# Kernel tuning notes

Measured on AMD Instinct MI355X. Metric: run time of the kernel, lower is better.

## Reference

```python
import jax, jax.numpy as jnp
import numpy as np

OUT, N_GROUPS, GROUP = 11008, 32, 128
IN = N_GROUPS * GROUP  # 4096
TOKENS = 2048


def setup_inputs() -> dict:
    key = jax.random.key(0)
    k_x, k_w, k_sc, k_s, k_b = jax.random.split(key, 5)
    x = jax.random.normal(k_x, (TOKENS, IN), dtype=jnp.float32)
    # quantized 4-bit signed weights in [-7, 7] (stored int8 in torch; int32 here)
    w_q = jax.random.randint(k_w, (OUT, N_GROUPS, GROUP), -7, 8, dtype=jnp.int32)
    # per-(out, group) positive scales, bounded away from zero like the clamp(min=1e-5)
    scales = jax.random.uniform(k_sc, (OUT, N_GROUPS, 1), dtype=jnp.float32, minval=1e-3, maxval=0.05)
    # smoothing vector: positive, bounded away from zero (it divides x)
    s = jax.random.uniform(k_s, (IN,), dtype=jnp.float32, minval=0.5, maxval=2.0)
    bias = jax.random.normal(k_b, (OUT,), dtype=jnp.float32)
    return {"x": x, "w_q": w_q, "scales": scales, "s": s, "bias": bias}


def reference(x, w_q, scales, s, bias):
    orig_dtype = x.dtype
    # group-wise dequant: [O, G, K] * [O, G, 1] -> [O, I]
    w_recon = (w_q.astype(jnp.float32) * scales).reshape(OUT, IN)
    x_f = x.astype(jnp.float32) / s  # smoothing-scale division
    y = x_f @ w_recon.T + bias
    return y.astype(orig_dtype)
```

## Files before the change

### kernel.cpp

```cpp
#include <hip/hip_runtime.h>
#include <hip/hip_bf16.h>

#define TOKENS  2048
#define IN_DIM  4096
#define OUT_DIM 11008
#define NGROUPS 32

#define BM 128
#define BN 128
#define BKB 128
#define THREADS 512
#define NKT   (IN_DIM / BKB)
#define BUFB  32768
#define BOFF  16384

#define PREPA_BLOCKS  TOKENS
#define PREPB_BLOCKS  (OUT_DIM * IN_DIM / 16 / 256)
#define PREPSC_BLOCKS (OUT_DIM * NGROUPS / 256)
#define PREP_GRID     (PREPA_BLOCKS + PREPB_BLOCKS + PREPSC_BLOCKS)

using f32x4  = __attribute__((ext_vector_type(4))) float;
using i32x4  = __attribute__((ext_vector_type(4))) int;
using bf16x8 = __attribute__((ext_vector_type(8))) short;

typedef __attribute__((address_space(3))) char as3c;

static __device__ __forceinline__ short f2bf(float f) {
    union { float f; unsigned u; } v; v.f = f;
    unsigned r = v.u + 0x7FFFu + ((v.u >> 16) & 1u);
    return (short)(r >> 16);
}

static __device__ __forceinline__ int pack4(int a, int b, int c, int d) {
    return (a & 255) | ((b & 255) << 8) | ((c & 255) << 16) | ((d & 255) << 24);
}

#define SB0 __builtin_amdgcn_sched_barrier(0)
#define LDSR(dst, addr)   asm volatile("ds_read_b128 %0, %1" : "=v"(dst) : "v"(addr))
#define WAITL(n) do { asm volatile("s_waitcnt lgkmcnt(" #n ")"); SB0; } while (0)
#define WAITV(n) do { asm volatile("s_waitcnt vmcnt(" #n ")");  SB0; } while (0)

__global__ __launch_bounds__(256) void prep_fused(
    const float* __restrict__ x, const int* __restrict__ wq,
    const float* __restrict__ scales, const float* __restrict__ s,
    char* __restrict__ Aq, float* __restrict__ sx,
    char* __restrict__ Bq, float* __restrict__ scT)
{
    __shared__ float wm[4];
    const int bid = blockIdx.x, t = threadIdx.x;

    if (bid < PREPA_BLOCKS) {
        const int row = bid;
        const float* xp = x + (size_t)row * IN_DIM + t * 16;
        const float* sp = s + t * 16;
        f32x4 v[4];
        float m = 0.f;
        #pragma unroll
        for (int q = 0; q < 4; ++q) {
            f32x4 xv = *(const f32x4*)(xp + q * 4);
            f32x4 sv = *(const f32x4*)(sp + q * 4);
            #pragma unroll
            for (int e = 0; e < 4; ++e) {
                v[q][e] = xv[e] / sv[e];
                m = fmaxf(m, fabsf(v[q][e]));
            }
        }
        #pragma unroll
        for (int off = 32; off; off >>= 1) m = fmaxf(m, __shfl_xor(m, off));
        if ((t & 63) == 0) wm[t >> 6] = m;
        __syncthreads();
        m = fmaxf(fmaxf(wm[0], wm[1]), fmaxf(wm[2], wm[3]));
        m = fmaxf(m, 1e-20f);
        const float inv = 127.0f / m;
        i32x4 pk;
        #pragma unroll
        for (int q = 0; q < 4; ++q)
            pk[q] = pack4((int)rintf(v[q][0] * inv), (int)rintf(v[q][1] * inv),
                          (int)rintf(v[q][2] * inv), (int)rintf(v[q][3] * inv));
        ((i32x4*)(Aq + (size_t)row * IN_DIM))[t] = pk;
        if (t == 0) sx[row] = m * (1.0f / 127.0f);
    } else if (bid < PREPA_BLOCKS + PREPB_BLOCKS) {
        const int idx = (bid - PREPA_BLOCKS) * 256 + t;
        const int* wp = wq + (size_t)idx * 16;
        i32x4 w0 = *(const i32x4*)wp, w1 = *(const i32x4*)(wp + 4);
        i32x4 w2 = *(const i32x4*)(wp + 8), w3 = *(const i32x4*)(wp + 12);
        i32x4 pk;
        pk[0] = pack4(w0[0], w0[1], w0[2], w0[3]);
        pk[1] = pack4(w1[0], w1[1], w1[2], w1[3]);
        pk[2] = pack4(w2[0], w2[1], w2[2], w2[3]);
        pk[3] = pack4(w3[0], w3[1], w3[2], w3[3]);
        ((i32x4*)Bq)[idx] = pk;
    } else {
        const int idx = (bid - PREPA_BLOCKS - PREPB_BLOCKS) * 256 + t;
        const int g = idx / OUT_DIM;
        const int o = idx - g * OUT_DIM;
        scT[idx] = scales[o * NGROUPS + g];
    }
}

__global__ __launch_bounds__(THREADS, 4) void awq_gemm_i8(
    const char* __restrict__ Aq, const char* __restrict__ Bq,
    const float* __restrict__ scT, const float* __restrict__ sx,
    const float* __restrict__ bias, float* __restrict__ out)
{
    const int rb = blockIdx.x;
    const int bm = (rb >> 3) & 15;
    const int bn = (((rb >> 3) >> 4) << 3) + (rb & 7);
    if (bn >= OUT_DIM / BN) return;

    __shared__ char smem[2 * BUFB];
    as3c* ldsb = (as3c*)smem;
    const unsigned lbase = (unsigned)(size_t)ldsb;

    const int tid  = threadIdx.x;
    const int lane = tid & 63;
    const int w    = tid >> 6;
    const int wr   = w >> 2;
    const int wc   = w & 3;
    const int fr   = lane & 15;
    const int fko  = lane >> 4;

    const int h7 = fr & 7;
    const unsigned swz0 = (unsigned)(((0 * 4 + fko) ^ h7) * 16);
    const unsigned swz1 = (unsigned)(((1 * 4 + fko) ^ h7) * 16);
    const unsigned aB0 = lbase + (wr * 64 + fr) * 128 + swz0;
    const unsigned aB1 = lbase + (wr * 64 + fr) * 128 + swz1;
    const unsigned bB0 = lbase + BOFF + (wc * 32 + fr) * 128 + swz0;
    const unsigned bB1 = lbase + BOFF + (wc * 32 + fr) * 128 + swz1;

    const int srow = tid >> 3;
    const int sg   = ((tid & 7) ^ (srow & 7)) * 16;
    const char* aSrc = Aq + (size_t)(bm * BM + srow) * IN_DIM + sg;
    const char* bSrc = Bq + (size_t)(bn * BN + srow) * IN_DIM + sg;

    const float* scp = scT + bn * BN + wc * 32 + fr;

#define STG_A(Q, KT, P) __builtin_amdgcn_global_load_lds( \
    (const __attribute__((address_space(1))) void*)(const void*)(aSrc + (size_t)((Q) * 64) * IN_DIM + (KT) * BKB), \
    (__attribute__((address_space(3))) void*)(ldsb + (P) * BUFB + (Q) * 8192 + tid * 16), 16, 0, 0)
#define STG_B(Q, KT, P) __builtin_amdgcn_global_load_lds( \
    (const __attribute__((address_space(1))) void*)(const void*)(bSrc + (size_t)((Q) * 64) * IN_DIM + (KT) * BKB), \
    (__attribute__((address_space(3))) void*)(ldsb + (P) * BUFB + BOFF + (Q) * 8192 + tid * 16), 16, 0, 0)

#define SCV_GLOAD(D0, D1, G) do { \
    asm volatile("global_load_dword %0, %1, off" : "=v"(D0) : "v"(scp + (size_t)(G) * OUT_DIM)); \
    asm volatile("global_load_dword %0, %1, off" : "=v"(D1) : "v"(scp + (size_t)(G) * OUT_DIM + 16)); \
    SB0; } while (0)

    f32x4 accf[4][2];
    #pragma unroll
    for (int i = 0; i < 4; ++i) {
        accf[i][0] = (f32x4){0.f, 0.f, 0.f, 0.f};
        accf[i][1] = (f32x4){0.f, 0.f, 0.f, 0.f};
    }

    float c0, c1, n0 = 0.f, n1 = 0.f;

    STG_A(0, 0, 0); STG_A(1, 0, 0); STG_B(0, 0, 0); STG_B(1, 0, 0);
    SCV_GLOAD(c0, c1, 0);
    STG_A(0, 1, 1); STG_A(1, 1, 1); STG_B(0, 1, 1); STG_B(1, 1, 1);
    WAITV(4);
    __builtin_amdgcn_s_barrier();
    SB0;

    for (int t = 0; t < NKT; ++t) {
        const int P = t & 1;
        const unsigned po = (unsigned)(P * BUFB);
        const bool haveN = (t + 1 < NKT);
        const bool haveS = (t + 2 < NKT);

        i32x4 a[4][2], b[2][2];
        LDSR(b[0][0], bB0 + po);        LDSR(b[0][1], bB1 + po);
        LDSR(b[1][0], bB0 + po + 2048); LDSR(b[1][1], bB1 + po + 2048);
        #pragma unroll
        for (int i = 0; i < 4; ++i) {
            LDSR(a[i][0], aB0 + po + i * 2048);
            LDSR(a[i][1], aB1 + po + i * 2048);
        }
        WAITL(0);
        __builtin_amdgcn_s_barrier();
        SB0;

        if (haveN) SCV_GLOAD(n0, n1, t + 1);
        if (haveS) { STG_A(0, t + 2, P); STG_A(1, t + 2, P);
                     STG_B(0, t + 2, P); STG_B(1, t + 2, P); }

        __builtin_amdgcn_s_setprio(1);
        #pragma unroll
        for (int i = 0; i < 4; ++i) {
            i32x4 t0 = __builtin_amdgcn_mfma_i32_16x16x64_i8(a[i][0], b[0][0], (i32x4){0,0,0,0}, 0, 0, 0);
            t0       = __builtin_amdgcn_mfma_i32_16x16x64_i8(a[i][1], b[0][1], t0, 0, 0, 0);
            i32x4 t1 = __builtin_amdgcn_mfma_i32_16x16x64_i8(a[i][0], b[1][0], (i32x4){0,0,0,0}, 0, 0, 0);
            t1       = __builtin_amdgcn_mfma_i32_16x16x64_i8(a[i][1], b[1][1], t1, 0, 0, 0);
            #pragma unroll
            for (int e = 0; e < 4; ++e) {
                accf[i][0][e] += (float)t0[e] * c0;
                accf[i][1][e] += (float)t1[e] * c1;
            }
        }
        __builtin_amdgcn_s_setprio(0);

        if (t < NKT - 2) { WAITV(4); } else { WAITV(0); }
        __builtin_amdgcn_s_barrier();
        SB0;
        if (haveN) { c0 = n0; c1 = n1; }
    }

    #pragma unroll
    for (int i = 0; i < 4; ++i) {
        const int row = bm * BM + wr * 64 + i * 16 + fko * 4;
        const f32x4 sxv = *(const f32x4*)(sx + row);
        #pragma unroll
        for (int j = 0; j < 2; ++j) {
            const int col = bn * BN + wc * 32 + j * 16 + fr;
            const float bv = bias[col];
            #pragma unroll
            for (int e = 0; e < 4; ++e)
                out[(size_t)(row + e) * OUT_DIM + col] = accf[i][j][e] * sxv[e] + bv;
        }
    }

#undef STG_A
#undef STG_B
#undef SCV_GLOAD
}

__global__ __launch_bounds__(256) void awq_gemm_fb(
    const float* __restrict__ x, const int* __restrict__ wq,
    const float* __restrict__ scales, const float* __restrict__ s,
    const float* __restrict__ bias, float* __restrict__ out)
{
    __shared__ short As[128][32];
    __shared__ short Bs[128][32];
    const int tid = threadIdx.x, lane = tid & 63, wave = tid >> 6;
    const int nbn = OUT_DIM / 128;
    const int bm = blockIdx.x / nbn, bn = blockIdx.x % nbn;
    const int srow = tid >> 1, scol = (tid & 1) * 16;
    const int wm = (wave >> 1) * 64, wn = (wave & 1) * 64;
    f32x4 acc[4][4];
    #pragma unroll
    for (int i = 0; i < 4; ++i)
        #pragma unroll
        for (int j = 0; j < 4; ++j) acc[i][j] = (f32x4){0.f, 0.f, 0.f, 0.f};
    const float* xrow = x + (size_t)(bm * 128 + srow) * IN_DIM;
    const int* wrow = wq + (size_t)(bn * 128 + srow) * IN_DIM;
    const float* scrow = scales + (size_t)(bn * 128 + srow) * NGROUPS;
    const int fr = lane & 15, fk = (lane >> 4) * 8, fq = lane >> 4;
    for (int kt = 0; kt < IN_DIM / 32; ++kt) {
        const int k0 = kt * 32;
        {
            const float* xp = xrow + k0 + scol;
            const float* sp = s + k0 + scol;
            short tmp[16];
            #pragma unroll
            for (int q = 0; q < 4; ++q) {
                f32x4 xv = *(const f32x4*)(xp + q * 4);
                f32x4 sv = *(const f32x4*)(sp + q * 4);
                #pragma unroll
                for (int e = 0; e < 4; ++e) tmp[q * 4 + e] = f2bf(xv[e] / sv[e]);
            }
            #pragma unroll
            for (int e = 0; e < 16; ++e) As[srow][scol + e] = tmp[e];
        }
        {
            const float sc = scrow[kt >> 2];
            const int* wp = wrow + k0 + scol;
            short tmp[16];
            #pragma unroll
            for (int q = 0; q < 4; ++q) {
                i32x4 wv = *(const i32x4*)(wp + q * 4);
                #pragma unroll
                for (int e = 0; e < 4; ++e) tmp[q * 4 + e] = f2bf((float)wv[e] * sc);
            }
            #pragma unroll
            for (int e = 0; e < 16; ++e) Bs[srow][scol + e] = tmp[e];
        }
        __syncthreads();
        bf16x8 a[4], b[4];
        #pragma unroll
        for (int i = 0; i < 4; ++i) a[i] = *(const bf16x8*)&As[wm + i * 16 + fr][fk];
        #pragma unroll
        for (int j = 0; j < 4; ++j) b[j] = *(const bf16x8*)&Bs[wn + j * 16 + fr][fk];
        #pragma unroll
        for (int i = 0; i < 4; ++i)
            #pragma unroll
            for (int j = 0; j < 4; ++j)
                acc[i][j] = __builtin_amdgcn_mfma_f32_16x16x32_bf16(a[i], b[j], acc[i][j], 0, 0, 0);
        __syncthreads();
    }
    #pragma unroll
    for (int i = 0; i < 4; ++i) {
        const int row = bm * 128 + wm + i * 16 + fq * 4;
        #pragma unroll
        for (int j = 0; j < 4; ++j) {
            const int col = bn * 128 + wn + j * 16 + fr;
            const float bv = bias[col];
            #pragma unroll
            for (int e = 0; e < 4; ++e)
                out[(size_t)(row + e) * OUT_DIM + col] = acc[i][j][e] + bv;
        }
    }
}

extern "C" void kernel_launch(void* const* d_in, const int* in_sizes, int n_in,
                              void* d_out, int out_size, void* d_ws, size_t ws_size,
                              hipStream_t stream) {
    const float* x      = (const float*)d_in[0];
    const int*   wq     = (const int*)  d_in[1];
    const float* scales = (const float*)d_in[2];
    const float* s      = (const float*)d_in[3];
    const float* bias   = (const float*)d_in[4];
    float* out = (float*)d_out;

    const size_t off_sx = (size_t)TOKENS * IN_DIM;
    const size_t off_bq = off_sx + 8192;
    const size_t off_sc = off_bq + (size_t)OUT_DIM * IN_DIM;
    const size_t need   = off_sc + (size_t)OUT_DIM * NGROUPS * 4;

    if (ws_size >= need) {
        char*  Aq  = (char*)d_ws;
        float* sxw = (float*)((char*)d_ws + off_sx);
        char*  Bq  = (char*)d_ws + off_bq;
        float* scT = (float*)((char*)d_ws + off_sc);
        prep_fused<<<PREP_GRID, 256, 0, stream>>>(x, wq, scales, s, Aq, sxw, Bq, scT);
        awq_gemm_i8<<<1408, THREADS, 0, stream>>>(Aq, Bq, scT, sxw, bias, out);
    } else {
        awq_gemm_fb<<<(TOKENS / 128) * (OUT_DIM / 128), 256, 0, stream>>>(x, wq, scales, s, bias, out);
    }
}
```

Measured before the change: 174.6 us.

## Use 256-thread blocks with 64x64 wave tiles and single-buffered LDS

Halves the block to four waves, so each wave now computes a 64x64 output sub-tile with four B fragments instead of two. This raises register-level reuse of the A fragments and cuts LDS reads per MFMA. LDS drops from a double buffer to a single 32KB buffer. The next tile is fetched straight into that buffer once the current tile is in registers, and a full vmcnt wait ends each iteration. The cost is a shallower prefetch pipeline and more accumulator registers per thread, with launch bounds lowered to 3 blocks.

```diff
diff --git a/kernel.cpp b/kernel.cpp
--- a/kernel.cpp
+++ b/kernel.cpp
@@ -9,7 +9,7 @@
 #define BM 128
 #define BN 128
 #define BKB 128
-#define THREADS 512
+#define THREADS 256
 #define NKT   (IN_DIM / BKB)
 #define BUFB  32768
 #define BOFF  16384
@@ -98,7 +98,7 @@
     }
 }
 
-__global__ __launch_bounds__(THREADS, 4) void awq_gemm_i8(
+__global__ __launch_bounds__(THREADS, 3) void awq_gemm_i8(
     const char* __restrict__ Aq, const char* __restrict__ Bq,
     const float* __restrict__ scT, const float* __restrict__ sx,
     const float* __restrict__ bias, float* __restrict__ out)
@@ -108,15 +108,15 @@
     const int bn = (((rb >> 3) >> 4) << 3) + (rb & 7);
     if (bn >= OUT_DIM / BN) return;
 
-    __shared__ char smem[2 * BUFB];
+    __shared__ char smem[BUFB];
     as3c* ldsb = (as3c*)smem;
     const unsigned lbase = (unsigned)(size_t)ldsb;
 
     const int tid  = threadIdx.x;
     const int lane = tid & 63;
     const int w    = tid >> 6;
-    const int wr   = w >> 2;
-    const int wc   = w & 3;
+    const int wr   = w >> 1;
+    const int wc   = w & 1;
     const int fr   = lane & 15;
     const int fko  = lane >> 4;
 
@@ -125,85 +125,89 @@
     const unsigned swz1 = (unsigned)(((1 * 4 + fko) ^ h7) * 16);
     const unsigned aB0 = lbase + (wr * 64 + fr) * 128 + swz0;
     const unsigned aB1 = lbase + (wr * 64 + fr) * 128 + swz1;
-    const unsigned bB0 = lbase + BOFF + (wc * 32 + fr) * 128 + swz0;
-    const unsigned bB1 = lbase + BOFF + (wc * 32 + fr) * 128 + swz1;
+    const unsigned bB0 = lbase + BOFF + (wc * 64 + fr) * 128 + swz0;
+    const unsigned bB1 = lbase + BOFF + (wc * 64 + fr) * 128 + swz1;
 
     const int srow = tid >> 3;
     const int sg   = ((tid & 7) ^ (srow & 7)) * 16;
     const char* aSrc = Aq + (size_t)(bm * BM + srow) * IN_DIM + sg;
     const char* bSrc = Bq + (size_t)(bn * BN + srow) * IN_DIM + sg;
 
-    const float* scp = scT + bn * BN + wc * 32 + fr;
-
-#define STG_A(Q, KT, P) __builtin_amdgcn_global_load_lds( \
-    (const __attribute__((address_space(1))) void*)(const void*)(aSrc + (size_t)((Q) * 64) * IN_DIM + (KT) * BKB), \
-    (__attribute__((address_space(3))) void*)(ldsb + (P) * BUFB + (Q) * 8192 + tid * 16), 16, 0, 0)
-#define STG_B(Q, KT, P) __builtin_amdgcn_global_load_lds( \
-    (const __attribute__((address_space(1))) void*)(const void*)(bSrc + (size_t)((Q) * 64) * IN_DIM + (KT) * BKB), \
-    (__attribute__((address_space(3))) void*)(ldsb + (P) * BUFB + BOFF + (Q) * 8192 + tid * 16), 16, 0, 0)
-
-#define SCV_GLOAD(D0, D1, G) do { \
-    asm volatile("global_load_dword %0, %1, off" : "=v"(D0) : "v"(scp + (size_t)(G) * OUT_DIM)); \
-    asm volatile("global_load_dword %0, %1, off" : "=v"(D1) : "v"(scp + (size_t)(G) * OUT_DIM + 16)); \
+    const float* scp = scT + bn * BN + wc * 64 + fr;
+
+#define STG_A(Q, KT) __builtin_amdgcn_global_load_lds( \
+    (const __attribute__((address_space(1))) void*)(const void*)(aSrc + (size_t)((Q) * 32) * IN_DIM + (KT) * BKB), \
+    (__attribute__((address_space(3))) void*)(ldsb + (Q) * 4096 + tid * 16), 16, 0, 0)
+#define STG_B(Q, KT) __builtin_amdgcn_global_load_lds( \
+    (const __attribute__((address_space(1))) void*)(const void*)(bSrc + (size_t)((Q) * 32) * IN_DIM + (KT) * BKB), \
+    (__attribute__((address_space(3))) void*)(ldsb + BOFF + (Q) * 4096 + tid * 16), 16, 0, 0)
+#define STG_TILE(KT) do { \
+    STG_A(0, KT); STG_A(1, KT); STG_A(2, KT); STG_A(3, KT); \
+    STG_B(0, KT); STG_B(1, KT); STG_B(2, KT); STG_B(3, KT); \
     SB0; } while (0)
 
-    f32x4 accf[4][2];
+#define SCV4(D0, D1, D2, D3, G) do { \
+    asm volatile("global_load_dword %0, %1, off"            : "=v"(D0) : "v"(scp + (size_t)(G) * OUT_DIM)); \
+    asm volatile("global_load_dword %0, %1, off offset:64"  : "=v"(D1) : "v"(scp + (size_t)(G) * OUT_DIM)); \
+    asm volatile("global_load_dword %0, %1, off offset:128" : "=v"(D2) : "v"(scp + (size_t)(G) * OUT_DIM)); \
+    asm volatile("global_load_dword %0, %1, off offset:192" : "=v"(D3) : "v"(scp + (size_t)(G) * OUT_DIM)); \
+    SB0; } while (0)
+
+#define QUADJ(J, CJ) do { \
+    _Pragma("unroll") \
+    for (int i = 0; i < 4; ++i) { \
+        i32x4 tq = __builtin_amdgcn_mfma_i32_16x16x64_i8(a[i][0], b[J][0], (i32x4){0,0,0,0}, 0, 0, 0); \
+        tq       = __builtin_amdgcn_mfma_i32_16x16x64_i8(a[i][1], b[J][1], tq, 0, 0, 0); \
+        _Pragma("unroll") \
+        for (int e = 0; e < 4; ++e) accf[i][J][e] += (float)tq[e] * (CJ); \
+    } } while (0)
+
+    f32x4 accf[4][4];
     #pragma unroll
-    for (int i = 0; i < 4; ++i) {
-        accf[i][0] = (f32x4){0.f, 0.f, 0.f, 0.f};
-        accf[i][1] = (f32x4){0.f, 0.f, 0.f, 0.f};
-    }
-
-    float c0, c1, n0 = 0.f, n1 = 0.f;
-
-    STG_A(0, 0, 0); STG_A(1, 0, 0); STG_B(0, 0, 0); STG_B(1, 0, 0);
-    SCV_GLOAD(c0, c1, 0);
-    STG_A(0, 1, 1); STG_A(1, 1, 1); STG_B(0, 1, 1); STG_B(1, 1, 1);
-    WAITV(4);
+    for (int i = 0; i < 4; ++i)
+        #pragma unroll
+        for (int j = 0; j < 4; ++j) accf[i][j] = (f32x4){0.f, 0.f, 0.f, 0.f};
+
+    float c0, c1, c2, c3, n0 = 0.f, n1 = 0.f, n2 = 0.f, n3 = 0.f;
+
+    STG_TILE(0);
+    SCV4(c0, c1, c2, c3, 0);
+    WAITV(0);
     __builtin_amdgcn_s_barrier();
     SB0;
 
     for (int t = 0; t < NKT; ++t) {
-        const int P = t & 1;
-        const unsigned po = (unsigned)(P * BUFB);
         const bool haveN = (t + 1 < NKT);
-        const bool haveS = (t + 2 < NKT);
-
-        i32x4 a[4][2], b[2][2];
-        LDSR(b[0][0], bB0 + po);        LDSR(b[0][1], bB1 + po);
-        LDSR(b[1][0], bB0 + po + 2048); LDSR(b[1][1], bB1 + po + 2048);
+
+        i32x4 a[4][2], b[4][2];
         #pragma unroll
         for (int i = 0; i < 4; ++i) {
-            LDSR(a[i][0], aB0 + po + i * 2048);
-            LDSR(a[i][1], aB1 + po + i * 2048);
+            LDSR(a[i][0], aB0 + i * 2048);
+            LDSR(a[i][1], aB1 + i * 2048);
+        }
+        #pragma unroll
+        for (int j = 0; j < 4; ++j) {
+            LDSR(b[j][0], bB0 + j * 2048);
+            LDSR(b[j][1], bB1 + j * 2048);
         }
         WAITL(0);
         __builtin_amdgcn_s_barrier();
         SB0;
 
-        if (haveN) SCV_GLOAD(n0, n1, t + 1);
-        if (haveS) { STG_A(0, t + 2, P); STG_A(1, t + 2, P);
-                     STG_B(0, t + 2, P); STG_B(1, t + 2, P); }
+        if (haveN) {
+            SCV4(n0, n1, n2, n3, t + 1);
+            STG_TILE(t + 1);
+        }
+        SB0;
 
         __builtin_amdgcn_s_setprio(1);
-        #pragma unroll
-        for (int i = 0; i < 4; ++i) {
-            i32x4 t0 = __builtin_amdgcn_mfma_i32_16x16x64_i8(a[i][0], b[0][0], (i32x4){0,0,0,0}, 0, 0, 0);
-            t0       = __builtin_amdgcn_mfma_i32_16x16x64_i8(a[i][1], b[0][1], t0, 0, 0, 0);
-            i32x4 t1 = __builtin_amdgcn_mfma_i32_16x16x64_i8(a[i][0], b[1][0], (i32x4){0,0,0,0}, 0, 0, 0);
-            t1       = __builtin_amdgcn_mfma_i32_16x16x64_i8(a[i][1], b[1][1], t1, 0, 0, 0);
-            #pragma unroll
-            for (int e = 0; e < 4; ++e) {
-                accf[i][0][e] += (float)t0[e] * c0;
-                accf[i][1][e] += (float)t1[e] * c1;
-            }
-        }
+        QUADJ(0, c0); QUADJ(1, c1); QUADJ(2, c2); QUADJ(3, c3);
         __builtin_amdgcn_s_setprio(0);
 
-        if (t < NKT - 2) { WAITV(4); } else { WAITV(0); }
+        WAITV(0);
         __builtin_amdgcn_s_barrier();
         SB0;
-        if (haveN) { c0 = n0; c1 = n1; }
+        if (haveN) { c0 = n0; c1 = n1; c2 = n2; c3 = n3; }
     }
 
     #pragma unroll
@@ -211,8 +215,8 @@
         const int row = bm * BM + wr * 64 + i * 16 + fko * 4;
         const f32x4 sxv = *(const f32x4*)(sx + row);
         #pragma unroll
-        for (int j = 0; j < 2; ++j) {
-            const int col = bn * BN + wc * 32 + j * 16 + fr;
+        for (int j = 0; j < 4; ++j) {
+            const int col = bn * BN + wc * 64 + j * 16 + fr;
             const float bv = bias[col];
             #pragma unroll
             for (int e = 0; e < 4; ++e)
@@ -222,7 +226,9 @@
 
 #undef STG_A
 #undef STG_B
-#undef SCV_GLOAD
+#undef STG_TILE
+#undef SCV4
+#undef QUADJ
 }
 
 __global__ __launch_bounds__(256) void awq_gemm_fb(
```

New measurement: 173.5 us, median of 3. About the same (-0.6%).
